# Optimization experiments

Measured on AMD Instinct MI355X. Metric: run time of the kernel, lower is better.

Reference implementation:

```python
import math
import jax, jax.numpy as jnp
import numpy as np

N, E, D, MSG, TDIM, H = 50000, 1000000, 128, 64, 32, 2
ED = MSG + TDIM  # edge_dim = 96


def setup_inputs() -> dict:
    key = jax.random.key(0)
    ks = jax.random.split(key, 32)
    f32 = jnp.float32
    nrm = lambda k, shp, s=1.0: jax.random.normal(k, shp, f32) * s
    x = nrm(ks[0], (N, D))
    last_update = jax.random.uniform(ks[1], (N,), f32, 0.0, 1000.0)
    edge_index = jax.random.randint(ks[2], (2, E), 0, N, dtype=jnp.int32)
    t = jax.random.uniform(ks[3], (E,), f32, 0.0, 1000.0)
    msg = nrm(ks[4], (E, MSG))
    s_in = 1.0 / math.sqrt(D)
    s_ed = 1.0 / math.sqrt(ED)
    def conv_params(kbase):
        kk = jax.random.split(kbase, 9)
        return dict(
            Wq=nrm(kk[0], (D, D), s_in), bq=jnp.zeros((D,), f32),
            Wk=nrm(kk[1], (D, D), s_in), bk=jnp.zeros((D,), f32),
            Wv=nrm(kk[2], (D, D), s_in), bv=jnp.zeros((D,), f32),
            We=nrm(kk[3], (ED, D), s_ed),  # lin_edge has no bias in PyG
            Ws=nrm(kk[4], (D, D), s_in), bs=jnp.zeros((D,), f32),
        )
    p1 = conv_params(ks[5])
    p2 = conv_params(ks[6])
    inp = {
        'x': x, 'last_update': last_update, 'edge_index': edge_index, 't': t, 'msg': msg,
        'time_w': nrm(ks[7], (TDIM,)), 'time_b': nrm(ks[8], (TDIM,), 0.1),
        'bn_g': jnp.ones((D,), f32), 'bn_b': jnp.zeros((D,), f32),
    }
    for name, p in (('1', p1), ('2', p2)):
        for k2, v2 in p.items():
            inp[k2 + name] = v2
    return inp


def _transformer_conv(h, edge_attr, src, dst, Wq, bq, Wk, bk, Wv, bv, We, Ws, bs):
    n = h.shape[0]
    C = Wq.shape[1] // H
    q = (h @ Wq + bq).reshape(n, H, C)
    k = (h @ Wk + bk).reshape(n, H, C)
    v = (h @ Wv + bv).reshape(n, H, C)
    e = (edge_attr @ We).reshape(-1, H, C)  # [E,H,C]
    kj = k[src] + e                           # key_j + edge
    alpha = jnp.einsum('ehc,ehc->eh', q[dst], kj) / jnp.sqrt(jnp.asarray(C, h.dtype))
    # segment softmax over destination neighborhoods (dropout omitted: eval mode)
    amax = jax.lax.stop_gradient(jax.ops.segment_max(alpha, dst, num_segments=n))
    ex = jnp.exp(alpha - amax[dst])
    den = jax.ops.segment_sum(ex, dst, num_segments=n)
    a = ex / den[dst]
    out = jax.ops.segment_sum((v[src] + e) * a[:, :, None], dst, num_segments=n)
    return out.reshape(n, H * C) + h @ Ws + bs  # concat heads + root skip


def reference(x, last_update, edge_index, t, msg, time_w, time_b,
              Wq1, bq1, Wk1, bk1, Wv1, bv1, We1, Ws1, bs1,
              Wq2, bq2, Wk2, bk2, Wv2, bv2, We2, Ws2, bs2,
              bn_g, bn_b):
    src, dst = edge_index[0], edge_index[1]
    rel_t = last_update[src] - t                       # [E]
    rel_t_enc = jnp.cos(rel_t[:, None] * time_w[None, :] + time_b)  # TGN TimeEncoder
    edge_attr = jnp.concatenate([rel_t_enc, msg], axis=-1)          # [E, 96]
    h = _transformer_conv(x, edge_attr, src, dst, Wq1, bq1, Wk1, bk1, Wv1, bv1, We1, Ws1, bs1)
    mu = h.mean(axis=0)
    var = ((h - mu) ** 2).mean(axis=0)  # biased var (torch BN training norm)
    h = (h - mu) / jnp.sqrt(var + 1e-5) * bn_g + bn_b
    h = jax.nn.relu(h)
    return _transformer_conv(h, edge_attr, src, dst, Wq2, bq2, Wk2, bk2, Wv2, bv2, We2, Ws2, bs2)
```

## Files before the change

kernel.cpp:

```cpp
#include <hip/hip_runtime.h>
#include <math.h>

#define DD 128
typedef unsigned short ushort_t;
typedef unsigned int uint_t;
typedef __attribute__((ext_vector_type(8))) short bf16x8;
typedef __attribute__((ext_vector_type(4))) float f32x4;

template<int CTRL>
__device__ __forceinline__ float dppAdd(float x) {
    int y = __builtin_amdgcn_update_dpp(0, __float_as_int(x), CTRL, 0xF, 0xF, true);
    return x + __int_as_float(y);
}
__device__ __forceinline__ float red16(float x) {
    x = dppAdd<0xB1>(x);
    x = dppAdd<0x4E>(x);
    x = dppAdd<0x141>(x);
    x = dppAdd<0x140>(x);
    return x;
}

__device__ __forceinline__ ushort_t f2bf(float f) {
    uint_t u = __float_as_uint(f);
    u += 0x7FFFu + ((u >> 16) & 1u);
    return (ushort_t)(u >> 16);
}
__device__ __forceinline__ uint_t packbf(float a, float b) {
    return (uint_t)f2bf(a) | ((uint_t)f2bf(b) << 16);
}
__device__ __forceinline__ float bflo(uint_t u) { return __uint_as_float(u << 16); }
__device__ __forceinline__ float bfhi(uint_t u) { return __uint_as_float(u & 0xFFFF0000u); }

__global__ __launch_bounds__(256) void hist_kernel(const int* __restrict__ ei,
                                                   int* __restrict__ cnt, int E) {
    int i = blockIdx.x * 256 + threadIdx.x;
    if (i < E) atomicAdd(&cnt[ei[E + i]], 1);
}

__global__ __launch_bounds__(1024) void scan_kernel(const int* __restrict__ cnt,
                                                    int* __restrict__ row_start,
                                                    int* __restrict__ cursor, int N) {
    __shared__ int part[1024];
    const int tid = threadIdx.x;
    const int chunk = (N + 1023) >> 10;
    const int lo = min(N, tid * chunk);
    const int hi = min(N, lo + chunk);
    int s = 0;
    for (int i = lo; i < hi; ++i) s += cnt[i];
    part[tid] = s;
    __syncthreads();
    for (int off = 1; off < 1024; off <<= 1) {
        int val = 0;
        if (tid >= off) val = part[tid - off];
        __syncthreads();
        part[tid] += val;
        __syncthreads();
    }
    int run = (tid == 0) ? 0 : part[tid - 1];
    for (int i = lo; i < hi; ++i) {
        row_start[i] = run; cursor[i] = run;
        run += cnt[i];
    }
    if (tid == 1023) row_start[N] = part[1023];
}

__global__ __launch_bounds__(256) void scatter_fb_kernel(
    const int* __restrict__ ei, const float* __restrict__ lu, const float* __restrict__ t,
    int* __restrict__ cursor, int4* __restrict__ ser, int E)
{
    int i = blockIdx.x * 256 + threadIdx.x;
    if (i < E) {
        int s = ei[i], d = ei[E + i];
        int pos = atomicAdd(&cursor[d], 1);
        ser[pos] = make_int4(s, i, __float_as_int(lu[s] - t[i]), 0);
    }
}

__global__ __launch_bounds__(256) void msg2bf_kernel(
    const float4* __restrict__ m4, uint2* __restrict__ o, size_t total4)
{
    size_t i = (size_t)blockIdx.x * 256 + threadIdx.x;
    const size_t stride = (size_t)gridDim.x * 256;
    for (; i < total4; i += stride) {
        float4 v = m4[i];
        o[i] = make_uint2(packbf(v.x, v.y), packbf(v.z, v.w));
    }
}

__global__ __launch_bounds__(256) void build_wu_kernel(
    const float* __restrict__ Wq, const float* __restrict__ bq,
    const float* __restrict__ We, float* __restrict__ Wu, float* __restrict__ bu)
{
    int idx = blockIdx.x * 256 + threadIdx.x;
    int h = idx >> 14;
    int r = (idx >> 7) & 127;
    int col = idx & 127;
    int lh = col >> 3, j = col & 7;
    int row = (j < 2) ? (2 * lh + j) : (j < 6 ? (32 + 4 * lh + (j - 2)) : -1);
    float s = 0.f, sb = 0.f;
    if (row >= 0) {
        for (int c = 0; c < 64; ++c) {
            float wv = We[row * 128 + h * 64 + c];
            s += Wq[r * 128 + h * 64 + c] * wv;
            if (r == 0) sb += bq[h * 64 + c] * wv;
        }
    }
    Wu[(h * 128 + r) * 128 + col] = s;
    if (r == 0) bu[h * 128 + col] = sb;
}

__global__ __launch_bounds__(256) void pack_w_kernel(
    const float* __restrict__ Wq, const float* __restrict__ Wk,
    const float* __restrict__ Wv, const float* __restrict__ Wsk,
    const float* __restrict__ Wu,
    const float* __restrict__ bq, const float* __restrict__ bk,
    const float* __restrict__ bv, const float* __restrict__ bsk,
    const float* __restrict__ bu,
    ushort_t* __restrict__ wcat, float* __restrict__ bcat)
{
    int idx = blockIdx.x * 256 + threadIdx.x;
    int cg = idx >> 7, k = idx & 127;
    int which = cg >> 7, col = cg & 127;
    float v, b;
    switch (which) {
        case 0:  v = Wq[k * 128 + col];          b = bq[col];       break;
        case 1:  v = Wk[k * 128 + col];          b = bk[col];       break;
        case 2:  v = Wv[k * 128 + col];          b = bv[col];       break;
        case 3:  v = Wsk[k * 128 + col];         b = bsk[col];      break;
        case 4:  v = Wu[k * 128 + col];          b = bu[col];       break;
        default: v = Wu[(128 + k) * 128 + col];  b = bu[128 + col]; break;
    }
    wcat[cg * 128 + k] = f2bf(v);
    if (k == 0) bcat[cg] = b;
}

__global__ __launch_bounds__(256) void mfma_gemm_kernel(
    const uint4* __restrict__ xb4,
    const uint4* __restrict__ wc4,
    const float* __restrict__ bcat,
    float* __restrict__ qb, ushort_t* __restrict__ kvbS,
    float* __restrict__ sb, float* __restrict__ ub, int M)
{
    __shared__ ushort_t Xs[64 * 136];
    __shared__ ushort_t Wt[128 * 136];
    const int tid = threadIdx.x;
    const int m0 = blockIdx.x * 64;
    const int cb = blockIdx.y;

    #pragma unroll
    for (int i = 0; i < 4; ++i) {
        int f = tid + i * 256, r = f >> 4, ch = f & 15;
        uint4 val = make_uint4(0, 0, 0, 0);
        if (m0 + r < M) val = xb4[(size_t)(m0 + r) * 16 + ch];
        *(uint4*)&Xs[r * 136 + ch * 8] = val;
    }
    #pragma unroll
    for (int i = 0; i < 8; ++i) {
        int f = tid + i * 256, r = f >> 4, ch = f & 15;
        *(uint4*)&Wt[r * 136 + ch * 8] = wc4[(size_t)(cb * 128 + r) * 16 + ch];
    }
    __syncthreads();

    const int w = tid >> 6, l = tid & 63, rl = l & 15, g = l >> 4;
    f32x4 acc[8];
    #pragma unroll
    for (int c = 0; c < 8; ++c) acc[c] = (f32x4){0.f, 0.f, 0.f, 0.f};
    const ushort_t* Ar = &Xs[(w * 16 + rl) * 136];
    #pragma unroll
    for (int kk = 0; kk < 4; ++kk) {
        bf16x8 a = *(const bf16x8*)&Ar[kk * 32 + g * 8];
        #pragma unroll
        for (int c = 0; c < 8; ++c) {
            bf16x8 b = *(const bf16x8*)&Wt[(c * 16 + rl) * 136 + kk * 32 + g * 8];
            acc[c] = __builtin_amdgcn_mfma_f32_16x16x32_bf16(a, b, acc[c], 0, 0, 0);
        }
    }
    float bias_c[8];
    #pragma unroll
    for (int c = 0; c < 8; ++c) bias_c[c] = bcat[cb * 128 + c * 16 + rl];

    float* fp = qb; int stride = 128, off = 0; bool isbf = false;
    switch (cb) {
        case 0: fp = qb; stride = 128; off = 0;   break;
        case 3: fp = sb; stride = 128; off = 0;   break;
        case 4: fp = ub; stride = 256; off = 0;   break;
        case 5: fp = ub; stride = 256; off = 128; break;
        case 1: isbf = true; off = 0;   break;
        default: isbf = true; off = 128; break;
    }
    const int R0 = m0 + w * 16 + g * 4;
    #pragma unroll
    for (int r = 0; r < 4; ++r) {
        int R = R0 + r;
        if (R < M) {
            if (isbf) {
                #pragma unroll
                for (int c = 0; c < 8; ++c)
                    kvbS[(size_t)R * 256 + off + c * 16 + rl] = f2bf(acc[c][r] + bias_c[c]);
            } else {
                #pragma unroll
                for (int c = 0; c < 8; ++c)
                    fp[(size_t)R * stride + off + c * 16 + rl] = acc[c][r] + bias_c[c];
            }
        }
    }
}

template<int PRE>
__global__ __launch_bounds__(256) void node_attn_kernel(
    const int* __restrict__ row_start, const int4* __restrict__ ser,
    const uint_t* __restrict__ eaB,
    const float* __restrict__ msg,
    const float* __restrict__ time_w, const float* __restrict__ time_b,
    const float* __restrict__ q, const uint_t* __restrict__ kvb,
    const float* __restrict__ u, float* __restrict__ nodeAcc, int N)
{
    const int tid = threadIdx.x;
    const int g = tid >> 5, l = tid & 31;
    const int lh = l & 15;
    const int h = l >> 4;
    const int n = blockIdx.x * 8 + g;
    if (n >= N) return;

    const float twA = time_w[2 * lh], twB = time_w[2 * lh + 1];
    const float tbA = time_b[2 * lh], tbB = time_b[2 * lh + 1];
    const int e0 = row_start[n], e1 = row_start[n + 1];
    const float4 q4 = ((const float4*)q)[(size_t)n * 32 + l];
    const float4 u0 = ((const float4*)u)[(size_t)n * 64 + h * 32 + lh * 2];
    const float4 u1 = ((const float4*)u)[(size_t)n * 64 + h * 32 + lh * 2 + 1];
    const uint2* KV2 = (const uint2*)kvb;
    const uint2* EB2 = (const uint2*)eaB;

    float4 wv = {0, 0, 0, 0};
    float sA = 0, sB = 0, s0 = 0, s1 = 0, s2 = 0, s3 = 0, den = 0;

    struct Ch { int src[4]; float rel[4]; uint2 eb[4]; float4 mf[4]; uint2 kk[4]; uint2 vv[4]; };
    Ch cur, nxt;

    auto LOAD_META = [&](Ch& c, int b) {
        #pragma unroll
        for (int j = 0; j < 4; ++j) {
            int idx = b + j; idx = idx < e1 ? idx : e1 - 1;
            int4 m = ser[idx];
            c.src[j] = m.x;
            c.rel[j] = __int_as_float(m.z);
            if (PRE) c.eb[j] = EB2[(size_t)m.y * 16 + lh];
            else     c.mf[j] = ((const float4*)msg)[(size_t)m.y * 16 + lh];
        }
    };
    auto LOAD_GATHER = [&](Ch& c) {
        #pragma unroll
        for (int j = 0; j < 4; ++j) {
            c.kk[j] = KV2[(size_t)c.src[j] * 64 + l];
            c.vv[j] = KV2[(size_t)c.src[j] * 64 + 32 + l];
        }
    };
    auto PROCESS = [&](Ch& c, int b) {
        #pragma unroll
        for (int j = 0; j < 4; ++j) {
            float cA = __cosf(c.rel[j] * twA + tbA);
            float cB = __cosf(c.rel[j] * twB + tbB);
            float m0, m1, m2, m3;
            if (PRE) {
                m0 = bflo(c.eb[j].x); m1 = bfhi(c.eb[j].x);
                m2 = bflo(c.eb[j].y); m3 = bfhi(c.eb[j].y);
            } else {
                m0 = c.mf[j].x; m1 = c.mf[j].y; m2 = c.mf[j].z; m3 = c.mf[j].w;
            }
            float k0 = bflo(c.kk[j].x), k1 = bfhi(c.kk[j].x);
            float k2 = bflo(c.kk[j].y), k3 = bfhi(c.kk[j].y);
            float p = q4.x * k0 + q4.y * k1 + q4.z * k2 + q4.w * k3
                    + cA * u0.x + cB * u0.y + m0 * u0.z + m1 * u0.w
                    + m2 * u1.x + m3 * u1.y;
            p = red16(p);
            float w = __expf(p * 0.125f);
            if (b + j >= e1) w = 0.f;
            den += w;
            float v0 = bflo(c.vv[j].x), v1 = bfhi(c.vv[j].x);
            float v2 = bflo(c.vv[j].y), v3 = bfhi(c.vv[j].y);
            wv.x += w * v0; wv.y += w * v1; wv.z += w * v2; wv.w += w * v3;
            sA += w * cA; sB += w * cB;
            s0 += w * m0; s1 += w * m1; s2 += w * m2; s3 += w * m3;
        }
    };

    if (e0 < e1) {
        LOAD_META(cur, e0);
        LOAD_GATHER(cur);
        for (int base = e0; base < e1; base += 4) {
            const bool more = (base + 4) < e1;
            if (more) LOAD_META(nxt, base + 4);
            PROCESS(cur, base);
            if (more) { LOAD_GATHER(nxt); cur = nxt; }
        }
    }
    float4* NA = (float4*)nodeAcc;
    NA[(size_t)n * 96 + l] = wv;
    NA[(size_t)n * 96 + 32 + l] = make_float4(sA, sB, s0, s1);
    NA[(size_t)n * 96 + 64 + l] = make_float4(s2, s3, den, 0.f);
}

__global__ __launch_bounds__(256) void ef_finish_kernel(
    const float* __restrict__ nodeAcc, const float* __restrict__ We,
    const float* __restrict__ sbuf, float* __restrict__ outp,
    float* __restrict__ bn_sum, float* __restrict__ bn_ssq, int N, int do_bn)
{
    __shared__ float seaL[16][2][100];
    __shared__ float denL[16][2];
    __shared__ float red[4][16][16];
    const int tid = threadIdx.x;
    const int n0 = blockIdx.x * 16;
    const float4* NA4 = (const float4*)nodeAcc;

    #pragma unroll
    for (int it = 0; it < 4; ++it) {
        int f = tid + it * 256;
        int i2 = f >> 6, s = f & 63;
        int lsub = s & 31, half = s >> 5;
        int h2 = lsub >> 4, lh2 = lsub & 15;
        float4 val = {0, 0, 0, 0};
        if (n0 + i2 < N) val = NA4[(size_t)(n0 + i2) * 96 + 32 + half * 32 + lsub];
        if (half == 0) {
            seaL[i2][h2][2 * lh2] = val.x;  seaL[i2][h2][2 * lh2 + 1] = val.y;
            seaL[i2][h2][32 + 4 * lh2] = val.z; seaL[i2][h2][32 + 4 * lh2 + 1] = val.w;
        } else {
            seaL[i2][h2][32 + 4 * lh2 + 2] = val.x; seaL[i2][h2][32 + 4 * lh2 + 3] = val.y;
            if (lh2 == 0) denL[i2][h2] = val.z;
        }
    }
    __syncthreads();

    const int i = tid >> 4, p = tid & 15, h = p >> 3;
    const int n = n0 + i;
    const float4* We4 = (const float4*)We;
    float4 a0 = {0, 0, 0, 0}, a1 = {0, 0, 0, 0};
    if (n < N) { a0 = NA4[(size_t)n * 96 + 2 * p]; a1 = NA4[(size_t)n * 96 + 2 * p + 1]; }
    #pragma unroll 8
    for (int j = 0; j < 96; ++j) {
        float sj = seaL[i][h][j];
        float4 w0 = We4[j * 32 + 2 * p], w1 = We4[j * 32 + 2 * p + 1];
        a0.x += sj * w0.x; a0.y += sj * w0.y; a0.z += sj * w0.z; a0.w += sj * w0.w;
        a1.x += sj * w1.x; a1.y += sj * w1.y; a1.z += sj * w1.z; a1.w += sj * w1.w;
    }
    float4 sk0 = {0, 0, 0, 0}, sk1 = {0, 0, 0, 0};
    if (n < N) {
        sk0 = ((const float4*)sbuf)[(size_t)n * 32 + 2 * p];
        sk1 = ((const float4*)sbuf)[(size_t)n * 32 + 2 * p + 1];
    }
    const float dn = denL[i][h];
    float4 o0, o1;
    if (dn > 0.f) {
        const float r = 1.0f / dn;
        o0.x = a0.x * r + sk0.x; o0.y = a0.y * r + sk0.y;
        o0.z = a0.z * r + sk0.z; o0.w = a0.w * r + sk0.w;
        o1.x = a1.x * r + sk1.x; o1.y = a1.y * r + sk1.y;
        o1.z = a1.z * r + sk1.z; o1.w = a1.w * r + sk1.w;
    } else { o0 = sk0; o1 = sk1; }
    if (n < N) {
        ((float4*)outp)[(size_t)n * 32 + 2 * p] = o0;
        ((float4*)outp)[(size_t)n * 32 + 2 * p + 1] = o1;
    }

    if (do_bn) {
        if (n >= N) { o0 = make_float4(0,0,0,0); o1 = make_float4(0,0,0,0); }
        auto rs = [&](float x, int c) {
            x += __shfl_xor(x, 16); x += __shfl_xor(x, 32);
            if ((tid & 63) < 16) red[tid >> 6][tid & 15][c] = x;
        };
        rs(o0.x, 0); rs(o0.y, 1); rs(o0.z, 2); rs(o0.w, 3);
        rs(o1.x, 4); rs(o1.y, 5); rs(o1.z, 6); rs(o1.w, 7);
        rs(o0.x * o0.x, 8);  rs(o0.y * o0.y, 9);  rs(o0.z * o0.z, 10); rs(o0.w * o0.w, 11);
        rs(o1.x * o1.x, 12); rs(o1.y * o1.y, 13); rs(o1.z * o1.z, 14); rs(o1.w * o1.w, 15);
        __syncthreads();
        int pp = tid >> 4, cc = tid & 15;
        float tot = red[0][pp][cc] + red[1][pp][cc] + red[2][pp][cc] + red[3][pp][cc];
        int ch = pp * 8 + (cc & 7);
        if (cc < 8) atomicAdd(&bn_sum[ch], tot);
        else        atomicAdd(&bn_ssq[ch], tot);
    }
}

__global__ void bn_stats_kernel(const float* __restrict__ bn_sum,
                                const float* __restrict__ bn_ssq,
                                float* __restrict__ mu, float* __restrict__ inv, int N)
{
    int c = threadIdx.x;
    float m = bn_sum[c] / (float)N;
    float var = bn_ssq[c] / (float)N - m * m;
    var = fmaxf(var, 0.f);
    mu[c] = m;
    inv[c] = rsqrtf(var + 1e-5f);
}

__global__ __launch_bounds__(256) void bn_apply_kernel(
    const float* __restrict__ pre, const float* __restrict__ mu,
    const float* __restrict__ inv, const float* __restrict__ gw,
    const float* __restrict__ bw, ushort_t* __restrict__ xb, size_t total)
{
    size_t i = (size_t)blockIdx.x * 256 + threadIdx.x;
    const size_t stride = (size_t)gridDim.x * 256;
    for (; i < total; i += stride) {
        int c = (int)(i & 127);
        float val = (pre[i] - mu[c]) * inv[c] * gw[c] + bw[c];
        xb[i] = f2bf(fmaxf(val, 0.f));
    }
}

extern "C" void kernel_launch(void* const* d_in, const int* in_sizes, int n_in,
                              void* d_out, int out_size, void* d_ws, size_t ws_size,
                              hipStream_t stream)
{
    const float* x   = (const float*)d_in[0];
    const float* lu  = (const float*)d_in[1];
    const int*   ei  = (const int*)d_in[2];
    const float* t   = (const float*)d_in[3];
    const float* msg = (const float*)d_in[4];
    const float* tw  = (const float*)d_in[5];
    const float* tb  = (const float*)d_in[6];
    const float* bng = (const float*)d_in[7];
    const float* bnb = (const float*)d_in[8];
    const float* Wq1 = (const float*)d_in[9];  const float* bq1 = (const float*)d_in[10];
    const float* Wk1 = (const float*)d_in[11]; const float* bk1 = (const float*)d_in[12];
    const float* Wv1 = (const float*)d_in[13]; const float* bv1 = (const float*)d_in[14];
    const float* We1 = (const float*)d_in[15];
    const float* Ws1 = (const float*)d_in[16]; const float* bs1 = (const float*)d_in[17];
    const float* Wq2 = (const float*)d_in[18]; const float* bq2 = (const float*)d_in[19];
    const float* Wk2 = (const float*)d_in[20]; const float* bk2 = (const float*)d_in[21];
    const float* Wv2 = (const float*)d_in[22]; const float* bv2 = (const float*)d_in[23];
    const float* We2 = (const float*)d_in[24];
    const float* Ws2 = (const float*)d_in[25]; const float* bs2 = (const float*)d_in[26];

    const int N = in_sizes[0] / DD;
    const int E = in_sizes[3];
    const size_t NM = (size_t)N * DD;

    float* f   = (float*)d_ws;
    float* qb  = f;
    float* sb  = qb + NM;
    float* ub  = sb + NM;
    float* pre = ub + 2 * NM;
    uint_t* kvb = (uint_t*)(pre + NM);
    ushort_t* xb = (ushort_t*)(kvb + (size_t)N * 128);
    float* nodeAcc = (float*)((char*)xb + (size_t)N * 128 * sizeof(ushort_t));
    ushort_t* wcat = (ushort_t*)(nodeAcc + (size_t)N * 384);
    float* bcat = (float*)(wcat + 98304);
    float* Wu  = bcat + 768;
    float* bu  = Wu + 32768;
    float* bsum = bu + 256;
    float* bssq = bsum + 128;
    float* muv  = bssq + 128;
    float* invv = muv + 128;
    int* cnt       = (int*)(invv + 128);
    int* row_start = cnt + N;
    int* cursor    = row_start + N + 1;
    char* tail0 = (char*)(cursor + N);
    size_t off = (((size_t)(tail0 - (char*)d_ws)) + 255) & ~(size_t)255;

    int4*   ser  = (int4*)((char*)d_ws + off);
    uint_t* eaB2 = (uint_t*)((char*)d_ws + off + (size_t)E * 16);
    size_t need_pre = off + (size_t)E * 16 + (size_t)E * 128 + 1024;
    const bool use_pre = (ws_size >= need_pre);

    const int EB = (E + 255) / 256;

    hipMemsetAsync(cnt, 0, (size_t)N * sizeof(int), stream);
    hist_kernel<<<EB, 256, 0, stream>>>(ei, cnt, E);
    scan_kernel<<<1, 1024, 0, stream>>>(cnt, row_start, cursor, N);
    scatter_fb_kernel<<<EB, 256, 0, stream>>>(ei, lu, t, cursor, ser, E);
    if (use_pre)
        msg2bf_kernel<<<4096, 256, 0, stream>>>(
            (const float4*)msg, (uint2*)eaB2, (size_t)E * 16);
    msg2bf_kernel<<<2048, 256, 0, stream>>>(
        (const float4*)x, (uint2*)xb, NM / 4);

    dim3 gemmGrid((N + 63) / 64, 6);
    const int attnGrid = (N + 7) / 8;
    const int finGrid = (N + 15) / 16;

    build_wu_kernel<<<128, 256, 0, stream>>>(Wq1, bq1, We1, Wu, bu);
    pack_w_kernel<<<384, 256, 0, stream>>>(
        Wq1, Wk1, Wv1, Ws1, Wu, bq1, bk1, bv1, bs1, bu, wcat, bcat);
    mfma_gemm_kernel<<<gemmGrid, 256, 0, stream>>>(
        (const uint4*)xb, (const uint4*)wcat, bcat,
        qb, (ushort_t*)kvb, sb, ub, N);
    if (use_pre)
        node_attn_kernel<1><<<attnGrid, 256, 0, stream>>>(
            row_start, ser, eaB2, msg, tw, tb, qb, kvb, ub, nodeAcc, N);
    else
        node_attn_kernel<0><<<attnGrid, 256, 0, stream>>>(
            row_start, ser, eaB2, msg, tw, tb, qb, kvb, ub, nodeAcc, N);
    hipMemsetAsync(bsum, 0, 256 * sizeof(float), stream);
    ef_finish_kernel<<<finGrid, 256, 0, stream>>>(
        nodeAcc, We1, sb, pre, bsum, bssq, N, 1);
    bn_stats_kernel<<<1, 128, 0, stream>>>(bsum, bssq, muv, invv, N);
    bn_apply_kernel<<<2048, 256, 0, stream>>>(pre, muv, invv, bng, bnb, xb, NM);

    build_wu_kernel<<<128, 256, 0, stream>>>(Wq2, bq2, We2, Wu, bu);
    pack_w_kernel<<<384, 256, 0, stream>>>(
        Wq2, Wk2, Wv2, Ws2, Wu, bq2, bk2, bv2, bs2, bu, wcat, bcat);
    mfma_gemm_kernel<<<gemmGrid, 256, 0, stream>>>(
        (const uint4*)xb, (const uint4*)wcat, bcat,
        qb, (ushort_t*)kvb, sb, ub, N);
    if (use_pre)
        node_attn_kernel<1><<<attnGrid, 256, 0, stream>>>(
            row_start, ser, eaB2, msg, tw, tb, qb, kvb, ub, nodeAcc, N);
    else
        node_attn_kernel<0><<<attnGrid, 256, 0, stream>>>(
            row_start, ser, eaB2, msg, tw, tb, qb, kvb, ub, nodeAcc, N);
    ef_finish_kernel<<<finGrid, 256, 0, stream>>>(
        nodeAcc, We2, sb, (float*)d_out, nullptr, nullptr, N, 0);
}
```

Baseline: 852.5 us.

## Deepen attention gather prefetch to three stages and store node accumulators as bf16

The node attention loop now rotates three edge-chunk buffers, so gathers are issued two chunks ahead instead of one and gather latency has more time to hide. The per-node intermediate accumulators (weighted V and edge-feature sums) are packed to bf16, and the softmax denominator goes to a separate fp32 array. The finish kernel is changed to read and unpack this layout. This cuts intermediate write/read traffic, at the cost of more registers in the attention kernel (possible occupancy loss) and bf16 rounding of the accumulated sums.

```diff
diff --git a/kernel.cpp b/kernel.cpp
--- a/kernel.cpp
+++ b/kernel.cpp
@@ -30,6 +30,8 @@
 }
 __device__ __forceinline__ float bflo(uint_t u) { return __uint_as_float(u << 16); }
 __device__ __forceinline__ float bfhi(uint_t u) { return __uint_as_float(u & 0xFFFF0000u); }
+
+#define NA_STRIDE 160
 
 __global__ __launch_bounds__(256) void hist_kernel(const int* __restrict__ ei,
                                                    int* __restrict__ cnt, int E) {
@@ -213,7 +215,8 @@
     const float* __restrict__ msg,
     const float* __restrict__ time_w, const float* __restrict__ time_b,
     const float* __restrict__ q, const uint_t* __restrict__ kvb,
-    const float* __restrict__ u, float* __restrict__ nodeAcc, int N)
+    const float* __restrict__ u, uint_t* __restrict__ nodeAccB,
+    float* __restrict__ denb, int N)
 {
     const int tid = threadIdx.x;
     const int g = tid >> 5, l = tid & 31;
@@ -232,10 +235,10 @@
     const uint2* EB2 = (const uint2*)eaB;
 
     float4 wv = {0, 0, 0, 0};
-    float sA = 0, sB = 0, s0 = 0, s1 = 0, s2 = 0, s3 = 0, den = 0;
+    float sA = 0, sB = 0, s0 = 0, s1 = 0, s2 = 0, s3 = 0, denA = 0;
 
     struct Ch { int src[4]; float rel[4]; uint2 eb[4]; float4 mf[4]; uint2 kk[4]; uint2 vv[4]; };
-    Ch cur, nxt;
+    Ch c0, c1, c2;
 
     auto LOAD_META = [&](Ch& c, int b) {
         #pragma unroll
@@ -275,7 +278,7 @@
             p = red16(p);
             float w = __expf(p * 0.125f);
             if (b + j >= e1) w = 0.f;
-            den += w;
+            denA += w;
             float v0 = bflo(c.vv[j].x), v1 = bfhi(c.vv[j].x);
             float v2 = bflo(c.vv[j].y), v3 = bfhi(c.vv[j].y);
             wv.x += w * v0; wv.y += w * v1; wv.z += w * v2; wv.w += w * v3;
@@ -285,47 +288,53 @@
     };
 
     if (e0 < e1) {
-        LOAD_META(cur, e0);
-        LOAD_GATHER(cur);
-        for (int base = e0; base < e1; base += 4) {
-            const bool more = (base + 4) < e1;
-            if (more) LOAD_META(nxt, base + 4);
-            PROCESS(cur, base);
-            if (more) { LOAD_GATHER(nxt); cur = nxt; }
-        }
-    }
-    float4* NA = (float4*)nodeAcc;
-    NA[(size_t)n * 96 + l] = wv;
-    NA[(size_t)n * 96 + 32 + l] = make_float4(sA, sB, s0, s1);
-    NA[(size_t)n * 96 + 64 + l] = make_float4(s2, s3, den, 0.f);
+        LOAD_META(c0, e0);
+        LOAD_GATHER(c0);
+        if (e0 + 4 < e1) { LOAD_META(c1, e0 + 4); LOAD_GATHER(c1); }
+        int base = e0;
+        auto STEP = [&](Ch& pc, Ch& fc) -> bool {
+            if (base >= e1) return false;
+            const bool more = (base + 8) < e1;
+            if (more) LOAD_META(fc, base + 8);
+            PROCESS(pc, base);
+            if (more) LOAD_GATHER(fc);
+            base += 4;
+            return true;
+        };
+        while (STEP(c0, c2) && STEP(c1, c0) && STEP(c2, c1)) {}
+    }
+    uint_t* NB = nodeAccB + (size_t)n * NA_STRIDE;
+    NB[2 * l]     = packbf(wv.x, wv.y);
+    NB[2 * l + 1] = packbf(wv.z, wv.w);
+    NB[64 + 3 * l]     = packbf(sA, sB);
+    NB[64 + 3 * l + 1] = packbf(s0, s1);
+    NB[64 + 3 * l + 2] = packbf(s2, s3);
+    if (lh == 0) denb[(size_t)n * 2 + h] = denA;
 }
 
 __global__ __launch_bounds__(256) void ef_finish_kernel(
-    const float* __restrict__ nodeAcc, const float* __restrict__ We,
+    const uint_t* __restrict__ nodeAccB, const float* __restrict__ denb,
+    const float* __restrict__ We,
     const float* __restrict__ sbuf, float* __restrict__ outp,
     float* __restrict__ bn_sum, float* __restrict__ bn_ssq, int N, int do_bn)
 {
     __shared__ float seaL[16][2][100];
-    __shared__ float denL[16][2];
     __shared__ float red[4][16][16];
     const int tid = threadIdx.x;
     const int n0 = blockIdx.x * 16;
-    const float4* NA4 = (const float4*)nodeAcc;
-
-    #pragma unroll
-    for (int it = 0; it < 4; ++it) {
+
+    #pragma unroll
+    for (int it = 0; it < 6; ++it) {
         int f = tid + it * 256;
-        int i2 = f >> 6, s = f & 63;
-        int lsub = s & 31, half = s >> 5;
-        int h2 = lsub >> 4, lh2 = lsub & 15;
-        float4 val = {0, 0, 0, 0};
-        if (n0 + i2 < N) val = NA4[(size_t)(n0 + i2) * 96 + 32 + half * 32 + lsub];
-        if (half == 0) {
-            seaL[i2][h2][2 * lh2] = val.x;  seaL[i2][h2][2 * lh2 + 1] = val.y;
-            seaL[i2][h2][32 + 4 * lh2] = val.z; seaL[i2][h2][32 + 4 * lh2 + 1] = val.w;
-        } else {
-            seaL[i2][h2][32 + 4 * lh2 + 2] = val.x; seaL[i2][h2][32 + 4 * lh2 + 3] = val.y;
-            if (lh2 == 0) denL[i2][h2] = val.z;
+        int i2 = f / 96, wi = f - i2 * 96;
+        if (n0 + i2 < N) {
+            uint_t uv = nodeAccB[(size_t)(n0 + i2) * NA_STRIDE + 64 + wi];
+            int L = wi / 3, k = wi - L * 3;
+            int h2 = L >> 4, lh2 = L & 15;
+            float lo = bflo(uv), hi = bfhi(uv);
+            if (k == 0)      { seaL[i2][h2][2 * lh2] = lo;         seaL[i2][h2][2 * lh2 + 1] = hi; }
+            else if (k == 1) { seaL[i2][h2][32 + 4 * lh2] = lo;    seaL[i2][h2][32 + 4 * lh2 + 1] = hi; }
+            else             { seaL[i2][h2][32 + 4 * lh2 + 2] = lo; seaL[i2][h2][32 + 4 * lh2 + 3] = hi; }
         }
     }
     __syncthreads();
@@ -333,28 +342,33 @@
     const int i = tid >> 4, p = tid & 15, h = p >> 3;
     const int n = n0 + i;
     const float4* We4 = (const float4*)We;
-    float4 a0 = {0, 0, 0, 0}, a1 = {0, 0, 0, 0};
-    if (n < N) { a0 = NA4[(size_t)n * 96 + 2 * p]; a1 = NA4[(size_t)n * 96 + 2 * p + 1]; }
+    float a[8] = {0, 0, 0, 0, 0, 0, 0, 0};
+    if (n < N) {
+        uint4 wu = *(const uint4*)&nodeAccB[(size_t)n * NA_STRIDE + 4 * p];
+        a[0] = bflo(wu.x); a[1] = bfhi(wu.x); a[2] = bflo(wu.y); a[3] = bfhi(wu.y);
+        a[4] = bflo(wu.z); a[5] = bfhi(wu.z); a[6] = bflo(wu.w); a[7] = bfhi(wu.w);
+    }
     #pragma unroll 8
     for (int j = 0; j < 96; ++j) {
         float sj = seaL[i][h][j];
         float4 w0 = We4[j * 32 + 2 * p], w1 = We4[j * 32 + 2 * p + 1];
-        a0.x += sj * w0.x; a0.y += sj * w0.y; a0.z += sj * w0.z; a0.w += sj * w0.w;
-        a1.x += sj * w1.x; a1.y += sj * w1.y; a1.z += sj * w1.z; a1.w += sj * w1.w;
+        a[0] += sj * w0.x; a[1] += sj * w0.y; a[2] += sj * w0.z; a[3] += sj * w0.w;
+        a[4] += sj * w1.x; a[5] += sj * w1.y; a[6] += sj * w1.z; a[7] += sj * w1.w;
     }
     float4 sk0 = {0, 0, 0, 0}, sk1 = {0, 0, 0, 0};
+    float dn = 0.f;
     if (n < N) {
         sk0 = ((const float4*)sbuf)[(size_t)n * 32 + 2 * p];
         sk1 = ((const float4*)sbuf)[(size_t)n * 32 + 2 * p + 1];
-    }
-    const float dn = denL[i][h];
+        dn = denb[(size_t)n * 2 + h];
+    }
     float4 o0, o1;
     if (dn > 0.f) {
         const float r = 1.0f / dn;
-        o0.x = a0.x * r + sk0.x; o0.y = a0.y * r + sk0.y;
-        o0.z = a0.z * r + sk0.z; o0.w = a0.w * r + sk0.w;
-        o1.x = a1.x * r + sk1.x; o1.y = a1.y * r + sk1.y;
-        o1.z = a1.z * r + sk1.z; o1.w = a1.w * r + sk1.w;
+        o0.x = a[0] * r + sk0.x; o0.y = a[1] * r + sk0.y;
+        o0.z = a[2] * r + sk0.z; o0.w = a[3] * r + sk0.w;
+        o1.x = a[4] * r + sk1.x; o1.y = a[5] * r + sk1.y;
+        o1.z = a[6] * r + sk1.z; o1.w = a[7] * r + sk1.w;
     } else { o0 = sk0; o1 = sk1; }
     if (n < N) {
         ((float4*)outp)[(size_t)n * 32 + 2 * p] = o0;
@@ -441,8 +455,9 @@
     float* pre = ub + 2 * NM;
     uint_t* kvb = (uint_t*)(pre + NM);
     ushort_t* xb = (ushort_t*)(kvb + (size_t)N * 128);
-    float* nodeAcc = (float*)((char*)xb + (size_t)N * 128 * sizeof(ushort_t));
-    ushort_t* wcat = (ushort_t*)(nodeAcc + (size_t)N * 384);
+    uint_t* nodeAccB = (uint_t*)((char*)xb + (size_t)N * 128 * sizeof(ushort_t));
+    float* denb = (float*)(nodeAccB + (size_t)N * NA_STRIDE);
+    ushort_t* wcat = (ushort_t*)(denb + (size_t)N * 2);
     float* bcat = (float*)(wcat + 98304);
     float* Wu  = bcat + 768;
     float* bu  = Wu + 32768;
@@ -485,13 +500,13 @@
         qb, (ushort_t*)kvb, sb, ub, N);
     if (use_pre)
         node_attn_kernel<1><<<attnGrid, 256, 0, stream>>>(
-            row_start, ser, eaB2, msg, tw, tb, qb, kvb, ub, nodeAcc, N);
+            row_start, ser, eaB2, msg, tw, tb, qb, kvb, ub, nodeAccB, denb, N);
     else
         node_attn_kernel<0><<<attnGrid, 256, 0, stream>>>(
-            row_start, ser, eaB2, msg, tw, tb, qb, kvb, ub, nodeAcc, N);
+            row_start, ser, eaB2, msg, tw, tb, qb, kvb, ub, nodeAccB, denb, N);
     hipMemsetAsync(bsum, 0, 256 * sizeof(float), stream);
     ef_finish_kernel<<<finGrid, 256, 0, stream>>>(
-        nodeAcc, We1, sb, pre, bsum, bssq, N, 1);
+        nodeAccB, denb, We1, sb, pre, bsum, bssq, N, 1);
     bn_stats_kernel<<<1, 128, 0, stream>>>(bsum, bssq, muv, invv, N);
     bn_apply_kernel<<<2048, 256, 0, stream>>>(pre, muv, invv, bng, bnb, xb, NM);
 
@@ -503,10 +518,10 @@
         qb, (ushort_t*)kvb, sb, ub, N);
     if (use_pre)
         node_attn_kernel<1><<<attnGrid, 256, 0, stream>>>(
-            row_start, ser, eaB2, msg, tw, tb, qb, kvb, ub, nodeAcc, N);
+            row_start, ser, eaB2, msg, tw, tb, qb, kvb, ub, nodeAccB, denb, N);
     else
         node_attn_kernel<0><<<attnGrid, 256, 0, stream>>>(
-            row_start, ser, eaB2, msg, tw, tb, qb, kvb, ub, nodeAcc, N);
+            row_start, ser, eaB2, msg, tw, tb, qb, kvb, ub, nodeAccB, denb, N);
     ef_finish_kernel<<<finGrid, 256, 0, stream>>>(
-        nodeAcc, We2, sb, (float*)d_out, nullptr, nullptr, N, 0);
-}
+        nodeAccB, denb, We2, sb, (float*)d_out, nullptr, nullptr, N, 0);
+}
```

After: 957.2 us. 12.3% more time.
